# Kernel tuning notes

Hardware: AMD Instinct MI355X
Metric: run time of the kernel (lower is better)

The kernel has to match this reference:

```python
import jax, jax.numpy as jnp
import numpy as np

N, E, L = 50000, 800000, 3
EPS = 1e-5


def mlp2(h, W1, b1, W2, b2):
    # Linear -> ReLU -> Linear
    return jax.nn.relu(h @ W1 + b1) @ W2 + b2


def setup_inputs() -> dict:
    key = jax.random.key(0)
    ks = jax.random.split(key, 20)
    s = 0.1  # weight scale to keep activations well-conditioned
    return {
        "x": jax.random.normal(ks[0], (N, 128), jnp.float32),
        "edge_attr": jax.random.normal(ks[1], (E, 64), jnp.float32),
        "edge_index": jax.random.randint(ks[2], (2, E), 0, N, dtype=jnp.int32),
        "Wn1": jax.random.normal(ks[3], (L, 128, 256), jnp.float32) * s,
        "bn1": jnp.zeros((L, 256), jnp.float32),
        "Wn2": jax.random.normal(ks[4], (L, 256, 128), jnp.float32) * s,
        "bn2": jnp.zeros((L, 128), jnp.float32),
        "We1": jax.random.normal(ks[5], (L, 64, 128), jnp.float32) * s,
        "be1": jnp.zeros((L, 128), jnp.float32),
        "We2": jax.random.normal(ks[6], (L, 128, 64), jnp.float32) * s,
        "be2": jnp.zeros((L, 64), jnp.float32),
        "Wm1": jax.random.normal(ks[7], (L, 320, 128), jnp.float32) * s,
        "bm1": jnp.zeros((L, 128), jnp.float32),
        "Wm2": jax.random.normal(ks[8], (L, 128, 128), jnp.float32) * s,
        "bm2": jnp.zeros((L, 128), jnp.float32),
        "lnw": jnp.ones((L, 128), jnp.float32),
        "lnb": jnp.zeros((L, 128), jnp.float32),
        "Wf": jax.random.normal(ks[9], (128, 64), jnp.float32) * s,
        "bf": jnp.zeros((64,), jnp.float32),
    }


def reference(x, edge_attr, edge_index, Wn1, bn1, Wn2, bn2, We1, be1, We2, be2,
              Wm1, bm1, Wm2, bm2, lnw, lnb, Wf, bf):
    src, dst = edge_index[0], edge_index[1]  # x_j = x[src], x_i = x[dst] (PyG source_to_target)
    deg = jax.ops.segment_sum(jnp.ones((E,), x.dtype), dst, num_segments=N)
    denom = jnp.maximum(deg, 1.0)[:, None]  # scatter-mean with clamp for isolated nodes
    for l in range(L):
        # mlp_node is the same function for x_i and x_j -> apply once per node, then gather
        xn = mlp2(x, Wn1[l], bn1[l], Wn2[l], bn2[l])        # [N, 128]
        e = mlp2(edge_attr, We1[l], be1[l], We2[l], be2[l])  # [E, 64]
        m = jnp.concatenate([xn[dst], xn[src], e], axis=-1)  # [E, 320] = [x_i, x_j, edge_attr]
        m = mlp2(m, Wm1[l], bm1[l], Wm2[l], bm2[l])          # [E, 128]
        agg = jax.ops.segment_sum(m, dst, num_segments=N) / denom  # mean aggregate [N, 128]
        mu = agg.mean(-1, keepdims=True)
        var = agg.var(-1, keepdims=True)
        h = (agg - mu) * jax.lax.rsqrt(var + EPS) * lnw[l] + lnb[l]  # LayerNorm
        x = jax.nn.relu(h)  # dropout p=0.0 -> identity
    return x @ Wf + bf  # jk='last' -> final linear on last layer output
```

## Files before the change

### kernel.cpp

```cpp
#include <hip/hip_runtime.h>
#include <stdint.h>

#define NN 50000
#define NE 800000
#define NB 196

typedef float f32x4 __attribute__((ext_vector_type(4)));
typedef short bf16x8 __attribute__((ext_vector_type(8)));

__device__ __forceinline__ unsigned short f2bf(float f) {
  union { float f; unsigned u; } v; v.f = f;
  unsigned r = v.u + 0x7fffu + ((v.u >> 16) & 1u);
  return (unsigned short)(r >> 16);
}
__device__ __forceinline__ float bf2f(unsigned short h) {
  union { unsigned u; float f; } v; v.u = ((unsigned)h) << 16;
  return v.f;
}
__device__ __forceinline__ float ldf(const void* p, size_t i, int m32) {
  return m32 ? ((const float*)p)[i] : bf2f(((const unsigned short*)p)[i]);
}

__global__ void detect_kernel(const void* lnw, int* flag) {
  if (threadIdx.x == 0 && blockIdx.x == 0)
    *flag = (((const unsigned short*)lnw)[0] == 0x3F80) ? 0 : 1;
}

#define oWn1 0
#define oWn2 98304
#define oWm1 196608
#define oWe1 319488
#define oWe2 344064
#define oWm2 368640
#define oWf  417792
#define NWTOT 425984
#define obn1 0
#define obn2 768
#define obe1 1152
#define obe2 1536
#define obm1 1728
#define obm2 2112
#define olnw 2496
#define olnb 2880
#define obf  3264
#define NBTOT 3328

__global__ __launch_bounds__(256) void conv_w(
    const void* Wn1, const void* Wn2, const void* Wm1, const void* We1,
    const void* We2, const void* Wm2, const void* Wf,
    const int* __restrict__ flg, unsigned short* __restrict__ cW)
{
  const int m32 = *flg;
  int i = blockIdx.x * 256 + threadIdx.x;
  if (i >= NWTOT) return;
  const void* src; size_t j;
  if      (i < oWn2) { src = Wn1; j = i - oWn1; }
  else if (i < oWm1) { src = Wn2; j = i - oWn2; }
  else if (i < oWe1) { src = Wm1; j = i - oWm1; }
  else if (i < oWe2) { src = We1; j = i - oWe1; }
  else if (i < oWm2) { src = We2; j = i - oWe2; }
  else if (i < oWf)  { src = Wm2; j = i - oWm2; }
  else               { src = Wf;  j = i - oWf;  }
  cW[i] = f2bf(ldf(src, j, m32));
}

__global__ __launch_bounds__(256) void conv_b(
    const void* bn1, const void* bn2, const void* be1, const void* be2,
    const void* bm1, const void* bm2, const void* lnw, const void* lnb,
    const void* bfv, const int* __restrict__ flg, float* __restrict__ cB)
{
  const int m32 = *flg;
  int i = blockIdx.x * 256 + threadIdx.x;
  if (i >= NBTOT) return;
  const void* src; size_t j;
  if      (i < obn2) { src = bn1; j = i - obn1; }
  else if (i < obe1) { src = bn2; j = i - obn2; }
  else if (i < obe2) { src = be1; j = i - obe1; }
  else if (i < obm1) { src = be2; j = i - obe2; }
  else if (i < obm2) { src = bm1; j = i - obm1; }
  else if (i < olnw) { src = bm2; j = i - obm2; }
  else if (i < olnb) { src = lnw; j = i - olnw; }
  else if (i < obf)  { src = lnb; j = i - olnb; }
  else               { src = bfv; j = i - obf;  }
  cB[i] = ldf(src, j, m32);
}

__global__ __launch_bounds__(256) void conv_x(const void* x, const int* flg,
                                              unsigned short* xc) {
  const int m32 = *flg;
  size_t i = (size_t)blockIdx.x * 256 + threadIdx.x;
  if (i < (size_t)NN * 128) xc[i] = f2bf(ldf(x, i, m32));
}

__global__ __launch_bounds__(256) void deg_int(const int* __restrict__ eidx,
                                               int* __restrict__ degi) {
  int i = blockIdx.x * 256 + threadIdx.x;
  if (i < NE) atomicAdd(degi + eidx[NE + i], 1);
}

__global__ __launch_bounds__(256) void scan1(const int* __restrict__ degi,
                                             int* __restrict__ base,
                                             int* __restrict__ bsum) {
  __shared__ int s[256];
  int t = threadIdx.x, i = blockIdx.x * 256 + t;
  int v = (i < NN) ? degi[i] : 0;
  s[t] = v; __syncthreads();
  for (int d = 1; d < 256; d <<= 1) {
    int u = (t >= d) ? s[t - d] : 0;
    __syncthreads();
    s[t] += u;
    __syncthreads();
  }
  if (i < NN) base[i] = s[t] - v;
  if (t == 255) bsum[blockIdx.x] = s[255];
}

__global__ void scan2(int* bsum) {
  __shared__ int s[256];
  int t = threadIdx.x;
  int v = (t < NB) ? bsum[t] : 0;
  s[t] = v; __syncthreads();
  for (int d = 1; d < 256; d <<= 1) {
    int u = (t >= d) ? s[t - d] : 0;
    __syncthreads();
    s[t] += u;
    __syncthreads();
  }
  if (t < NB) bsum[t] = s[t] - v;
}

__global__ __launch_bounds__(256) void scan3(int* base, const int* bsum) {
  int i = blockIdx.x * 256 + threadIdx.x;
  if (i < NN) base[i] += bsum[blockIdx.x];
}

__global__ __launch_bounds__(256) void scatter_sort(
    const int* __restrict__ eidx, const int* __restrict__ base,
    int* __restrict__ cursor, int* __restrict__ sE) {
  int e = blockIdx.x * 256 + threadIdx.x;
  if (e < NE) {
    int d = eidx[NE + e];
    int r = atomicAdd(cursor + d, 1);
    sE[base[d] + r] = e;
  }
}

__global__ __launch_bounds__(256) void prep_wc(
    const unsigned short* __restrict__ cW, const float* __restrict__ cB,
    float* __restrict__ Wc, float* __restrict__ bc2)
{
  int l = blockIdx.x;
  const unsigned short* We2l = cW + oWe2 + l * 8192;
  const unsigned short* Wm1c = cW + oWm1 + l * 40960 + 256 * 128;
  const float* be2l = cB + obe2 + l * 64;
  const float* bm1l = cB + obm1 + l * 128;
  float* out = Wc + l * 16384;
  for (int i = threadIdx.x; i < 16384; i += 256) {
    int k = i >> 7, n = i & 127;
    float s = 0.f;
    for (int u = 0; u < 64; u++)
      s += bf2f(We2l[k * 64 + u]) * bf2f(Wm1c[u * 128 + n]);
    out[i] = s;
  }
  if (threadIdx.x < 128) {
    int n = threadIdx.x;
    float s = bm1l[n];
    for (int u = 0; u < 64; u++)
      s += bf2f(be2l[u]) * bf2f(Wm1c[u * 128 + n]);
    bc2[l * 128 + n] = s;
  }
}

__global__ __launch_bounds__(256) void pack_frags(
    const unsigned short* __restrict__ cW, const float* __restrict__ Wcp,
    unsigned short* __restrict__ Wn1p, unsigned short* __restrict__ Wn2p,
    unsigned short* __restrict__ Wm1p, unsigned short* __restrict__ We1p,
    unsigned short* __restrict__ Wcpk)
{
  int l = blockIdx.x / 5, which = blockIdx.x % 5;
  int K, N, total;
  const unsigned short* src = nullptr;
  const float* srcf = nullptr;
  unsigned short* dst;
  if (which == 0)      { K = 128; N = 256; src = cW + oWn1 + (size_t)l * 32768; dst = Wn1p + (size_t)l * 32768; }
  else if (which == 1) { K = 256; N = 128; src = cW + oWn2 + (size_t)l * 32768; dst = Wn2p + (size_t)l * 32768; }
  else if (which == 2) { K = 128; N = 256; src = cW + oWm1 + (size_t)l * 40960; dst = Wm1p + (size_t)l * 32768; }
  else if (which == 3) { K = 64;  N = 128; src = cW + oWe1 + (size_t)l * 8192;  dst = We1p + (size_t)l * 8192; }
  else                 { K = 128; N = 128; srcf = Wcp + (size_t)l * 16384;      dst = Wcpk + (size_t)l * 16384; }
  int KB = K >> 5;
  total = K * N;
  for (int o = threadIdx.x; o < total; o += 256) {
    int j = o & 7, lane = (o >> 3) & 63, q = o >> 9;
    int kb = q % KB, c = q / KB;
    int k = kb * 32 + (lane >> 4) * 8 + j;
    int n = c * 16 + (lane & 15);
    unsigned short v;
    if (which == 2) {
      v = (n < 128) ? src[k * 128 + n] : src[(128 + k) * 128 + (n - 128)];
    } else if (which == 4) {
      v = f2bf(srcf[k * 128 + n]);
    } else {
      v = src[k * N + n];
    }
    dst[o] = v;
  }
}

__global__ __launch_bounds__(256) void node_p_mfma(
    const unsigned short* __restrict__ xin,
    const unsigned short* __restrict__ Wn1p, const unsigned short* __restrict__ Wn2p,
    const unsigned short* __restrict__ Wm1p, const float* __restrict__ cB,
    unsigned short* __restrict__ P, int l)
{
  __shared__ __align__(16) short HS[4][16 * 256];
  const int tid = threadIdx.x;
  const int wid = tid >> 6, lane = tid & 63, rl = lane & 15, cg = lane >> 4;
  const int n0 = blockIdx.x * 64;
  short* Hw = &HS[wid][0];
  const int swr = (rl & 7) << 3;

  int nA = n0 + wid * 16 + rl;
  int nAc = (nA < NN) ? nA : (NN - 1);

  bf16x8 ax[4];
  {
    const unsigned short* xr = xin + (size_t)nAc * 128;
    #pragma unroll
    for (int kb = 0; kb < 4; kb++)
      ax[kb] = *(const bf16x8*)&xr[kb * 32 + cg * 8];
  }

  {
    const unsigned short* Wb = Wn1p + (size_t)l * 32768;
    const float* b1 = cB + obn1 + l * 256;
    #pragma unroll
    for (int c = 0; c < 16; c++) {
      f32x4 acc = {0.f, 0.f, 0.f, 0.f};
      #pragma unroll
      for (int kb = 0; kb < 4; kb++) {
        bf16x8 b = *(const bf16x8*)&Wb[(size_t)(c * 4 + kb) * 512 + lane * 8];
        acc = __builtin_amdgcn_mfma_f32_16x16x32_bf16(ax[kb], b, acc, 0, 0, 0);
      }
      int col = c * 16 + rl;
      float bb = b1[col];
      #pragma unroll
      for (int r = 0; r < 4; r++) {
        int row = cg * 4 + r;
        Hw[row * 256 + (col ^ ((row & 7) << 3))] =
            (short)f2bf(fmaxf(acc[r] + bb, 0.f));
      }
    }
  }

  {
    bf16x8 ah[8];
    #pragma unroll
    for (int kb = 0; kb < 8; kb++)
      ah[kb] = *(const bf16x8*)&Hw[rl * 256 + ((kb * 32 + cg * 8) ^ swr)];
    const unsigned short* Wb = Wn2p + (size_t)l * 32768;
    const float* b2 = cB + obn2 + l * 128;
    #pragma unroll
    for (int c = 0; c < 8; c++) {
      f32x4 acc = {0.f, 0.f, 0.f, 0.f};
      #pragma unroll
      for (int kb = 0; kb < 8; kb++) {
        bf16x8 b = *(const bf16x8*)&Wb[(size_t)(c * 8 + kb) * 512 + lane * 8];
        acc = __builtin_amdgcn_mfma_f32_16x16x32_bf16(ah[kb], b, acc, 0, 0, 0);
      }
      int col = c * 16 + rl;
      float bb = b2[col];
      #pragma unroll
      for (int r = 0; r < 4; r++) {
        int row = cg * 4 + r;
        Hw[row * 128 + (col ^ ((row & 7) << 3))] = (short)f2bf(acc[r] + bb);
      }
    }
  }

  {
    bf16x8 an[4];
    #pragma unroll
    for (int kb = 0; kb < 4; kb++)
      an[kb] = *(const bf16x8*)&Hw[rl * 128 + ((kb * 32 + cg * 8) ^ swr)];
    const unsigned short* Wb = Wm1p + (size_t)l * 32768;
    #pragma unroll
    for (int c = 0; c < 16; c++) {
      f32x4 acc = {0.f, 0.f, 0.f, 0.f};
      #pragma unroll
      for (int kb = 0; kb < 4; kb++) {
        bf16x8 b = *(const bf16x8*)&Wb[(size_t)(c * 4 + kb) * 512 + lane * 8];
        acc = __builtin_amdgcn_mfma_f32_16x16x32_bf16(an[kb], b, acc, 0, 0, 0);
      }
      int col = c * 16 + rl;
      #pragma unroll
      for (int r = 0; r < 4; r++) {
        int row = cg * 4 + r;
        int n = n0 + wid * 16 + row;
        if (n < NN) P[(size_t)n * 256 + col] = f2bf(acc[r]);
      }
    }
  }
}

__global__ __launch_bounds__(256) void edge_fold_fused(
    const void* __restrict__ ea, const int* __restrict__ eidx,
    const int* __restrict__ sE, const int* __restrict__ baseg,
    const int* __restrict__ degg,
    const unsigned short* __restrict__ We1p, const unsigned short* __restrict__ Wcpk,
    const float* __restrict__ cB, const float* __restrict__ bc2,
    const unsigned short* __restrict__ P, float* __restrict__ agg,
    const int* __restrict__ flg, int l)
{
  __shared__ __align__(16) char SB[64 * 132 * 4];
  __shared__ int dstS[64], srcS[64];
  float* hS = (float*)SB;
  const int m32 = *flg;
  const int tid = threadIdx.x;
  const int wid = tid >> 6, lane = tid & 63, rl = lane & 15, cg = lane >> 4;
  const int e0 = blockIdx.x * 64;
  short* Rw = (short*)(SB + wid * 4096);
  const int swr = (rl & 7) << 3;

  const int brow = wid * 16 + rl;
  int eidA = sE[e0 + brow];
  if (cg == 0) {
    srcS[brow] = eidx[eidA];
    dstS[brow] = eidx[NE + eidA];
  }
  bf16x8 a0, a1;
  if (m32) {
    const float* er = (const float*)ea + (size_t)eidA * 64;
    f32x4 u0 = *(const f32x4*)&er[cg * 8];
    f32x4 u1 = *(const f32x4*)&er[cg * 8 + 4];
    f32x4 u2 = *(const f32x4*)&er[32 + cg * 8];
    f32x4 u3 = *(const f32x4*)&er[32 + cg * 8 + 4];
    alignas(16) unsigned short t0[8], t1[8];
    #pragma unroll
    for (int j = 0; j < 4; j++) {
      t0[j] = f2bf(u0[j]); t0[4 + j] = f2bf(u1[j]);
      t1[j] = f2bf(u2[j]); t1[4 + j] = f2bf(u3[j]);
    }
    a0 = *(const bf16x8*)t0; a1 = *(const bf16x8*)t1;
  } else {
    const unsigned short* er = (const unsigned short*)ea + (size_t)eidA * 64;
    a0 = *(const bf16x8*)&er[cg * 8];
    a1 = *(const bf16x8*)&er[32 + cg * 8];
  }

  {
    const unsigned short* Wb = We1p + (size_t)l * 8192;
    const float* be1l = cB + obe1 + l * 128;
    #pragma unroll
    for (int c = 0; c < 8; c++) {
      bf16x8 b0 = *(const bf16x8*)&Wb[(c * 2 + 0) * 512 + lane * 8];
      bf16x8 b1 = *(const bf16x8*)&Wb[(c * 2 + 1) * 512 + lane * 8];
      f32x4 acc = {0.f, 0.f, 0.f, 0.f};
      acc = __builtin_amdgcn_mfma_f32_16x16x32_bf16(a0, b0, acc, 0, 0, 0);
      acc = __builtin_amdgcn_mfma_f32_16x16x32_bf16(a1, b1, acc, 0, 0, 0);
      int col = c * 16 + rl;
      float b = be1l[col];
      #pragma unroll
      for (int r = 0; r < 4; r++) {
        int row = cg * 4 + r;
        Rw[row * 128 + (col ^ ((row & 7) << 3))] =
            (short)f2bf(fmaxf(acc[r] + b, 0.f));
      }
    }
  }

  f32x4 acc2[8];
  {
    bf16x8 ra[4];
    #pragma unroll
    for (int kb = 0; kb < 4; kb++)
      ra[kb] = *(const bf16x8*)&Rw[rl * 128 + ((kb * 32 + cg * 8) ^ swr)];
    const unsigned short* Wb = Wcpk + (size_t)l * 16384;
    #pragma unroll
    for (int c = 0; c < 8; c++) {
      f32x4 acc = {0.f, 0.f, 0.f, 0.f};
      #pragma unroll
      for (int kb = 0; kb < 4; kb++) {
        bf16x8 b = *(const bf16x8*)&Wb[(c * 4 + kb) * 512 + lane * 8];
        acc = __builtin_amdgcn_mfma_f32_16x16x32_bf16(ra[kb], b, acc, 0, 0, 0);
      }
      acc2[c] = acc;
    }
  }

  __syncthreads();

  #pragma unroll
  for (int c = 0; c < 8; c++) {
    int col = c * 16 + rl;
    #pragma unroll
    for (int r = 0; r < 4; r++) {
      int row = wid * 16 + cg * 4 + r;
      hS[row * 132 + col] = acc2[c][r];
    }
  }
  __syncthreads();

  {
    const int colg = tid & 15;
    const int rc = tid >> 4;
    const float* bc2l = bc2 + l * 128 + colg * 8;
    float bcv[8];
    #pragma unroll
    for (int j = 0; j < 8; j++) bcv[j] = bc2l[j];
    #pragma unroll
    for (int rr = 0; rr < 4; rr++) {
      int row = rc * 4 + rr;
      int di = dstS[row], si = srcS[row];
      float* hp = hS + row * 132 + colg * 8;
      f32x4 h0 = *(const f32x4*)hp;
      f32x4 h1 = *(const f32x4*)(hp + 4);
      bf16x8 pd = *(const bf16x8*)(P + (size_t)di * 256 + colg * 8);
      bf16x8 ps = *(const bf16x8*)(P + (size_t)si * 256 + 128 + colg * 8);
      #pragma unroll
      for (int j = 0; j < 4; j++) {
        h0[j] = fmaxf(h0[j] + bcv[j] + bf2f((unsigned short)pd[j]) +
                      bf2f((unsigned short)ps[j]), 0.f);
        h1[j] = fmaxf(h1[j] + bcv[4 + j] + bf2f((unsigned short)pd[4 + j]) +
                      bf2f((unsigned short)ps[4 + j]), 0.f);
      }
      *(f32x4*)hp = h0;
      *(f32x4*)(hp + 4) = h1;
    }
  }
  __syncthreads();

  if (tid < 128) {
    const int col = tid;
    float run = 0.f;
    int cur = dstS[0];
    for (int i = 0; i < 64; i++) {
      int d = dstS[i];
      if (d != cur) {
        int b0 = baseg[cur], dg = degg[cur];
        if (b0 >= e0 && b0 + dg <= e0 + 64)
          agg[(size_t)cur * 128 + col] = run;
        else
          atomicAdd(agg + (size_t)cur * 128 + col, run);
        run = 0.f; cur = d;
      }
      run += hS[i * 132 + col];
    }
    int b0 = baseg[cur], dg = degg[cur];
    if (b0 >= e0 && b0 + dg <= e0 + 64)
      agg[(size_t)cur * 128 + col] = run;
    else
      atomicAdd(agg + (size_t)cur * 128 + col, run);
  }
}

__global__ __launch_bounds__(256) void agg_w_ln(
    const float* __restrict__ aggH, const int* __restrict__ degi,
    const unsigned short* __restrict__ cW, const float* __restrict__ cB,
    unsigned short* __restrict__ xnext, int l)
{
  __shared__ float at[8][128];
  __shared__ float vs[8][128];
  const int tid = threadIdx.x;
  const int n0 = blockIdx.x * 8;
  for (int i = tid; i < 1024; i += 256) {
    int j = i >> 7, k = i & 127;
    int n = n0 + j;
    int d = degi[n];
    at[j][k] = aggH[(size_t)n * 128 + k] / (float)(d > 0 ? d : 1);
  }
  __syncthreads();
  {
    const int t = tid & 127, grp = tid >> 7;
    float acc[4] = {0.f, 0.f, 0.f, 0.f};
    const unsigned short* W = cW + oWm2 + (size_t)l * 16384 + t;
    for (int k = 0; k < 128; k += 4) {
      float w0 = bf2f(W[(k + 0) * 128]);
      float w1 = bf2f(W[(k + 1) * 128]);
      float w2 = bf2f(W[(k + 2) * 128]);
      float w3 = bf2f(W[(k + 3) * 128]);
      #pragma unroll
      for (int j = 0; j < 4; j++) {
        f32x4 v = *(const f32x4*)&at[grp * 4 + j][k];
        acc[j] += v[0] * w0 + v[1] * w1 + v[2] * w2 + v[3] * w3;
      }
    }
    float bm = cB[obm2 + l * 128 + t];
    #pragma unroll
    for (int j = 0; j < 4; j++) {
      int n = n0 + grp * 4 + j;
      vs[grp * 4 + j][t] = acc[j] + (degi[n] > 0 ? bm : 0.f);
    }
  }
  __syncthreads();
  const int w = tid >> 6, lane = tid & 63;
  float lw0 = cB[olnw + l * 128 + lane], lb0 = cB[olnb + l * 128 + lane];
  float lw1 = cB[olnw + l * 128 + lane + 64], lb1 = cB[olnb + l * 128 + lane + 64];
  #pragma unroll
  for (int jj = 0; jj < 2; jj++) {
    int j = w * 2 + jj;
    float v0 = vs[j][lane], v1 = vs[j][lane + 64];
    float s = v0 + v1, q = v0 * v0 + v1 * v1;
    #pragma unroll
    for (int m = 1; m < 64; m <<= 1) {
      s += __shfl_xor(s, m, 64);
      q += __shfl_xor(q, m, 64);
    }
    float mu = s * (1.f / 128.f);
    float var = fmaxf(q * (1.f / 128.f) - mu * mu, 0.f);
    float rs = rsqrtf(var + 1e-5f);
    int n = n0 + j;
    xnext[(size_t)n * 128 + lane] = f2bf(fmaxf((v0 - mu) * rs * lw0 + lb0, 0.f));
    xnext[(size_t)n * 128 + lane + 64] = f2bf(fmaxf((v1 - mu) * rs * lw1 + lb1, 0.f));
  }
}

__global__ __launch_bounds__(256) void final_k(
    const unsigned short* __restrict__ xc, const unsigned short* __restrict__ cW,
    const float* __restrict__ cB, const int* __restrict__ flg,
    void* __restrict__ out)
{
  const int m32 = *flg;
  const int tid = threadIdx.x;
  const int t = tid & 63;
  const int nd = blockIdx.x * 4 + (tid >> 6);
  float acc = cB[obf + t];
  const unsigned short* xr = xc + (size_t)nd * 128;
  const unsigned short* W = cW + oWf + t;
  for (int k = 0; k < 128; k++)
    acc += bf2f(xr[k]) * bf2f(W[(size_t)k * 64]);
  if (m32) ((float*)out)[(size_t)nd * 64 + t] = acc;
  else ((unsigned short*)out)[(size_t)nd * 64 + t] = f2bf(acc);
}

extern "C" void kernel_launch(void* const* d_in, const int* in_sizes, int n_in,
                              void* d_out, int out_size, void* d_ws, size_t ws_size,
                              hipStream_t stream) {
  (void)in_sizes; (void)n_in; (void)out_size; (void)ws_size;
  const void* x    = d_in[0];
  const void* ea   = d_in[1];
  const int*  eidx = (const int*)d_in[2];
  const void* Wn1  = d_in[3];
  const void* bn1  = d_in[4];
  const void* Wn2  = d_in[5];
  const void* bn2  = d_in[6];
  const void* We1  = d_in[7];
  const void* be1  = d_in[8];
  const void* We2  = d_in[9];
  const void* be2  = d_in[10];
  const void* Wm1  = d_in[11];
  const void* bm1  = d_in[12];
  const void* Wm2  = d_in[13];
  const void* bm2  = d_in[14];
  const void* lnw  = d_in[15];
  const void* lnb  = d_in[16];
  const void* Wf   = d_in[17];
  const void* bfv  = d_in[18];

  char* ws = (char*)d_ws;
  size_t off = 0;
  auto alloc = [&](size_t bytes) {
    size_t o = off;
    off += (bytes + 255) & ~(size_t)255;
    return o;
  };
  int*            flag = (int*)(ws + alloc(4));
  unsigned short* xcur = (unsigned short*)(ws + alloc((size_t)NN * 128 * 2));
  unsigned short* Pb   = (unsigned short*)(ws + alloc((size_t)NN * 256 * 2));
  float*          aggH = (float*)(ws + alloc((size_t)NN * 128 * 4));
  unsigned short* cW   = (unsigned short*)(ws + alloc((size_t)NWTOT * 2));
  float*          cB   = (float*)(ws + alloc((size_t)NBTOT * 4));
  float*          Wcp  = (float*)(ws + alloc(3 * 16384 * 4));
  float*          bc2w = (float*)(ws + alloc(3 * 128 * 4));
  unsigned short* We1p = (unsigned short*)(ws + alloc(3 * 8192 * 2));
  unsigned short* Wcpk = (unsigned short*)(ws + alloc(3 * 16384 * 2));
  unsigned short* Wn1p = (unsigned short*)(ws + alloc(3 * 32768 * 2));
  unsigned short* Wn2p = (unsigned short*)(ws + alloc(3 * 32768 * 2));
  unsigned short* Wm1p = (unsigned short*)(ws + alloc(3 * 32768 * 2));
  int*            degi = (int*)(ws + alloc((size_t)NN * 4));
  int*            baseb= (int*)(ws + alloc((size_t)NN * 4));
  int*            bsum = (int*)(ws + alloc(256 * 4));
  int*            curs = (int*)(ws + alloc((size_t)NN * 4));
  int*            sE   = (int*)(ws + alloc((size_t)NE * 4));

  detect_kernel<<<1, 64, 0, stream>>>(lnw, flag);
  conv_w<<<(NWTOT + 255) / 256, 256, 0, stream>>>(Wn1, Wn2, Wm1, We1, We2, Wm2,
                                                  Wf, flag, cW);
  conv_b<<<(NBTOT + 255) / 256, 256, 0, stream>>>(bn1, bn2, be1, be2, bm1, bm2,
                                                  lnw, lnb, bfv, flag, cB);
  conv_x<<<(NN * 128 + 255) / 256, 256, 0, stream>>>(x, flag, xcur);

  hipMemsetAsync(degi, 0, (size_t)NN * 4, stream);
  deg_int<<<(NE + 255) / 256, 256, 0, stream>>>(eidx, degi);
  scan1<<<NB, 256, 0, stream>>>(degi, baseb, bsum);
  scan2<<<1, 256, 0, stream>>>(bsum);
  scan3<<<NB, 256, 0, stream>>>(baseb, bsum);
  hipMemsetAsync(curs, 0, (size_t)NN * 4, stream);
  scatter_sort<<<(NE + 255) / 256, 256, 0, stream>>>(eidx, baseb, curs, sE);

  prep_wc<<<3, 256, 0, stream>>>(cW, cB, Wcp, bc2w);
  pack_frags<<<15, 256, 0, stream>>>(cW, Wcp, Wn1p, Wn2p, Wm1p, We1p, Wcpk);

  for (int l = 0; l < 3; l++) {
    node_p_mfma<<<(NN + 63) / 64, 256, 0, stream>>>(xcur, Wn1p, Wn2p, Wm1p,
                                                    cB, Pb, l);
    hipMemsetAsync(aggH, 0, (size_t)NN * 128 * 4, stream);
    edge_fold_fused<<<NE / 64, 256, 0, stream>>>(ea, eidx, sE, baseb, degi,
                                                 We1p, Wcpk, cB, bc2w, Pb,
                                                 aggH, flag, l);
    agg_w_ln<<<NN / 8, 256, 0, stream>>>(aggH, degi, cW, cB, xcur, l);
  }
  final_k<<<NN / 4, 256, 0, stream>>>(xcur, cW, cB, flag, d_out);
}
```

Measured before the change: 1.591 ms.

## Pre-gather sorted edge attributes and indices once; shrink edge kernel shared memory

Sorted src/dst indices and bf16 edge attributes are materialized once in dst-sorted order, so the three per-layer edge kernels read them contiguously instead of doing an indirect gather through sE. The edge kernel stores intermediate messages as bf16 in a smaller shared buffer, fuses the bias+P gather+ReLU into the register epilogue (dropping one sync pass), and requests higher occupancy via launch bounds. This costs an extra one-time gather kernel and about 100 MB of workspace. It also rounds messages to bf16 before aggregation, which loses some precision.

```diff
diff --git a/kernel.cpp b/kernel.cpp
--- a/kernel.cpp
+++ b/kernel.cpp
@@ -136,12 +136,37 @@
 
 __global__ __launch_bounds__(256) void scatter_sort(
     const int* __restrict__ eidx, const int* __restrict__ base,
-    int* __restrict__ cursor, int* __restrict__ sE) {
+    int* __restrict__ cursor, int* __restrict__ sE,
+    int* __restrict__ sSrc, int* __restrict__ sDst) {
   int e = blockIdx.x * 256 + threadIdx.x;
   if (e < NE) {
-    int d = eidx[NE + e];
+    int s = eidx[e], d = eidx[NE + e];
     int r = atomicAdd(cursor + d, 1);
-    sE[base[d] + r] = e;
+    int pos = base[d] + r;
+    sE[pos] = e; sSrc[pos] = s; sDst[pos] = d;
+  }
+}
+
+__global__ __launch_bounds__(256) void gather_ea(
+    const void* __restrict__ ea, const int* __restrict__ sE,
+    const int* __restrict__ flg, unsigned short* __restrict__ eaS) {
+  const int m32 = *flg;
+  int slot = blockIdx.x * 32 + (threadIdx.x >> 3);
+  int j = threadIdx.x & 7;
+  if (slot >= NE) return;
+  int eid = sE[slot];
+  unsigned short* dst = eaS + (size_t)slot * 64 + j * 8;
+  if (m32) {
+    const float* src = (const float*)ea + (size_t)eid * 64 + j * 8;
+    f32x4 v0 = *(const f32x4*)src;
+    f32x4 v1 = *(const f32x4*)(src + 4);
+    alignas(16) unsigned short t[8];
+    #pragma unroll
+    for (int q = 0; q < 4; q++) { t[q] = f2bf(v0[q]); t[4 + q] = f2bf(v1[q]); }
+    *(bf16x8*)dst = *(const bf16x8*)t;
+  } else {
+    const unsigned short* src = (const unsigned short*)ea + (size_t)eid * 64 + j * 8;
+    *(bf16x8*)dst = *(const bf16x8*)src;
   }
 }
 
@@ -302,50 +327,36 @@
   }
 }
 
-__global__ __launch_bounds__(256) void edge_fold_fused(
-    const void* __restrict__ ea, const int* __restrict__ eidx,
-    const int* __restrict__ sE, const int* __restrict__ baseg,
-    const int* __restrict__ degg,
+__global__ __launch_bounds__(256, 8) void edge_fold_v4(
+    const unsigned short* __restrict__ eaS,
+    const int* __restrict__ sSrc, const int* __restrict__ sDst,
+    const int* __restrict__ baseg, const int* __restrict__ degg,
     const unsigned short* __restrict__ We1p, const unsigned short* __restrict__ Wcpk,
     const float* __restrict__ cB, const float* __restrict__ bc2,
-    const unsigned short* __restrict__ P, float* __restrict__ agg,
-    const int* __restrict__ flg, int l)
-{
-  __shared__ __align__(16) char SB[64 * 132 * 4];
-  __shared__ int dstS[64], srcS[64];
-  float* hS = (float*)SB;
-  const int m32 = *flg;
+    const unsigned short* __restrict__ P, float* __restrict__ agg, int l)
+{
+  __shared__ __align__(16) short hS[64 * 136];
+  __shared__ int dstS[64];
   const int tid = threadIdx.x;
   const int wid = tid >> 6, lane = tid & 63, rl = lane & 15, cg = lane >> 4;
   const int e0 = blockIdx.x * 64;
-  short* Rw = (short*)(SB + wid * 4096);
+  short* Rw = hS + wid * 2048;
   const int swr = (rl & 7) << 3;
-
   const int brow = wid * 16 + rl;
-  int eidA = sE[e0 + brow];
-  if (cg == 0) {
-    srcS[brow] = eidx[eidA];
-    dstS[brow] = eidx[NE + eidA];
-  }
-  bf16x8 a0, a1;
-  if (m32) {
-    const float* er = (const float*)ea + (size_t)eidA * 64;
-    f32x4 u0 = *(const f32x4*)&er[cg * 8];
-    f32x4 u1 = *(const f32x4*)&er[cg * 8 + 4];
-    f32x4 u2 = *(const f32x4*)&er[32 + cg * 8];
-    f32x4 u3 = *(const f32x4*)&er[32 + cg * 8 + 4];
-    alignas(16) unsigned short t0[8], t1[8];
-    #pragma unroll
-    for (int j = 0; j < 4; j++) {
-      t0[j] = f2bf(u0[j]); t0[4 + j] = f2bf(u1[j]);
-      t1[j] = f2bf(u2[j]); t1[4 + j] = f2bf(u3[j]);
-    }
-    a0 = *(const bf16x8*)t0; a1 = *(const bf16x8*)t1;
-  } else {
-    const unsigned short* er = (const unsigned short*)ea + (size_t)eidA * 64;
-    a0 = *(const bf16x8*)&er[cg * 8];
-    a1 = *(const bf16x8*)&er[32 + cg * 8];
-  }
+
+  if (cg == 0) dstS[brow] = sDst[e0 + brow];
+
+  int di[4], si[4];
+  #pragma unroll
+  for (int r = 0; r < 4; r++) {
+    int row = e0 + wid * 16 + cg * 4 + r;
+    di[r] = sDst[row];
+    si[r] = sSrc[row];
+  }
+
+  const unsigned short* er = eaS + (size_t)(e0 + brow) * 64;
+  bf16x8 a0 = *(const bf16x8*)&er[cg * 8];
+  bf16x8 a1 = *(const bf16x8*)&er[32 + cg * 8];
 
   {
     const unsigned short* Wb = We1p + (size_t)l * 8192;
@@ -389,42 +400,20 @@
 
   __syncthreads();
 
-  #pragma unroll
-  for (int c = 0; c < 8; c++) {
-    int col = c * 16 + rl;
-    #pragma unroll
-    for (int r = 0; r < 4; r++) {
-      int row = wid * 16 + cg * 4 + r;
-      hS[row * 132 + col] = acc2[c][r];
-    }
-  }
-  __syncthreads();
-
-  {
-    const int colg = tid & 15;
-    const int rc = tid >> 4;
-    const float* bc2l = bc2 + l * 128 + colg * 8;
-    float bcv[8];
-    #pragma unroll
-    for (int j = 0; j < 8; j++) bcv[j] = bc2l[j];
-    #pragma unroll
-    for (int rr = 0; rr < 4; rr++) {
-      int row = rc * 4 + rr;
-      int di = dstS[row], si = srcS[row];
-      float* hp = hS + row * 132 + colg * 8;
-      f32x4 h0 = *(const f32x4*)hp;
-      f32x4 h1 = *(const f32x4*)(hp + 4);
-      bf16x8 pd = *(const bf16x8*)(P + (size_t)di * 256 + colg * 8);
-      bf16x8 ps = *(const bf16x8*)(P + (size_t)si * 256 + 128 + colg * 8);
-      #pragma unroll
-      for (int j = 0; j < 4; j++) {
-        h0[j] = fmaxf(h0[j] + bcv[j] + bf2f((unsigned short)pd[j]) +
-                      bf2f((unsigned short)ps[j]), 0.f);
-        h1[j] = fmaxf(h1[j] + bcv[4 + j] + bf2f((unsigned short)pd[4 + j]) +
-                      bf2f((unsigned short)ps[4 + j]), 0.f);
-      }
-      *(f32x4*)hp = h0;
-      *(f32x4*)(hp + 4) = h1;
+  {
+    const float* bc2l = bc2 + l * 128;
+    #pragma unroll
+    for (int c = 0; c < 8; c++) {
+      int col = c * 16 + rl;
+      float bv = bc2l[col];
+      #pragma unroll
+      for (int r = 0; r < 4; r++) {
+        int row = wid * 16 + cg * 4 + r;
+        float h = acc2[c][r] + bv
+                + bf2f(P[(size_t)di[r] * 256 + col])
+                + bf2f(P[(size_t)si[r] * 256 + 128 + col]);
+        hS[row * 136 + col] = (short)f2bf(fmaxf(h, 0.f));
+      }
     }
   }
   __syncthreads();
@@ -443,7 +432,7 @@
           atomicAdd(agg + (size_t)cur * 128 + col, run);
         run = 0.f; cur = d;
       }
-      run += hS[i * 132 + col];
+      run += bf2f((unsigned short)hS[i * 136 + col]);
     }
     int b0 = baseg[cur], dg = degg[cur];
     if (b0 >= e0 && b0 + dg <= e0 + 64)
@@ -581,6 +570,9 @@
   int*            bsum = (int*)(ws + alloc(256 * 4));
   int*            curs = (int*)(ws + alloc((size_t)NN * 4));
   int*            sE   = (int*)(ws + alloc((size_t)NE * 4));
+  int*            sSrc = (int*)(ws + alloc((size_t)NE * 4));
+  int*            sDst = (int*)(ws + alloc((size_t)NE * 4));
+  unsigned short* eaS  = (unsigned short*)(ws + alloc((size_t)NE * 64 * 2));
 
   detect_kernel<<<1, 64, 0, stream>>>(lnw, flag);
   conv_w<<<(NWTOT + 255) / 256, 256, 0, stream>>>(Wn1, Wn2, Wm1, We1, We2, Wm2,
@@ -595,7 +587,9 @@
   scan2<<<1, 256, 0, stream>>>(bsum);
   scan3<<<NB, 256, 0, stream>>>(baseb, bsum);
   hipMemsetAsync(curs, 0, (size_t)NN * 4, stream);
-  scatter_sort<<<(NE + 255) / 256, 256, 0, stream>>>(eidx, baseb, curs, sE);
+  scatter_sort<<<(NE + 255) / 256, 256, 0, stream>>>(eidx, baseb, curs, sE,
+                                                     sSrc, sDst);
+  gather_ea<<<NE / 32, 256, 0, stream>>>(ea, sE, flag, eaS);
 
   prep_wc<<<3, 256, 0, stream>>>(cW, cB, Wcp, bc2w);
   pack_frags<<<15, 256, 0, stream>>>(cW, Wcp, Wn1p, Wn2p, Wm1p, We1p, Wcpk);
@@ -604,9 +598,9 @@
     node_p_mfma<<<(NN + 63) / 64, 256, 0, stream>>>(xcur, Wn1p, Wn2p, Wm1p,
                                                     cB, Pb, l);
     hipMemsetAsync(aggH, 0, (size_t)NN * 128 * 4, stream);
-    edge_fold_fused<<<NE / 64, 256, 0, stream>>>(ea, eidx, sE, baseb, degi,
-                                                 We1p, Wcpk, cB, bc2w, Pb,
-                                                 aggH, flag, l);
+    edge_fold_v4<<<NE / 64, 256, 0, stream>>>(eaS, sSrc, sDst, baseb, degi,
+                                              We1p, Wcpk, cB, bc2w, Pb,
+                                              aggH, l);
     agg_w_ln<<<NN / 8, 256, 0, stream>>>(aggH, degi, cW, cB, xcur, l);
   }
   final_k<<<NN / 4, 256, 0, stream>>>(xcur, cW, cB, flag, d_out);
```

Result: faster. 1.548 ms (-2.7%).
